# Kernel tuning notes

Hardware: AMD Instinct MI355X
Metric: run time of the kernel (lower is better)

The kernel has to match this reference:

```python
import jax, jax.numpy as jnp
import numpy as np

N_CLUSTERS = 64
MAX_ITER = 10
TOL = 1e-4


def _dists(X, C):
    """Euclidean distance matrix, shape (K, N) — mirrors torch.cdist(centroids, X, 2)."""
    x2 = jnp.sum(X * X, axis=1)            # (N,)
    c2 = jnp.sum(C * C, axis=1)            # (K,)
    d2 = c2[:, None] + x2[None, :] - 2.0 * (C @ X.T)
    return jnp.sqrt(jnp.maximum(d2, 0.0))


def _init_centroids(X):
    """KMeans++-style farthest-point init: seed with X[0], then repeatedly add the
    point farthest from the current centroid set (mirrors centroids_init)."""
    K = N_CLUSTERS
    C0 = jnp.zeros((K, X.shape[1]), X.dtype).at[0].set(X[0])

    def body(C, i):
        valid = jnp.arange(K) < i                      # slots filled so far
        d = jnp.where(valid[:, None], _dists(X, C), jnp.inf)
        min_d = jnp.min(d, axis=0)                     # dist to nearest centroid
        idx = jnp.argmax(min_d)                        # farthest point = outlier
        return C.at[i].set(X[idx]), None

    C, _ = jax.lax.scan(body, C0, jnp.arange(1, K))
    return C


def _kmeans(X):
    K = N_CLUSTERS
    C = _init_centroids(X)
    ones = jnp.ones((X.shape[0],), X.dtype)

    def step(carry, _):
        C, done = carry
        lbl = jnp.argmin(_dists(X, C), axis=0)                       # (N,)
        counts = jax.ops.segment_sum(ones, lbl, num_segments=K)      # (K,)
        sums = jax.ops.segment_sum(X, lbl, num_segments=K)           # (K, D)
        means = sums / jnp.maximum(counts, 1.0)[:, None]
        empty = counts == 0
        # Empty cluster -> re-seed with farthest point from the kept means
        # (mirrors dropping NaN rows + centroids_init re-adding an outlier).
        dm = jnp.where(empty[:, None], jnp.inf, _dists(X, means))
        far = jnp.argmax(jnp.min(dm, axis=0))
        newC = jnp.where(empty[:, None], X[far], means)
        # Shift computed only over used (non-empty) centroids, as in calc_centr_shift.
        shift = jnp.sum(jnp.where(empty[:, None], 0.0, (means - C) ** 2))
        converged = (shift <= TOL) & (~jnp.any(empty))
        newC = jnp.where(done, C, newC)                              # freeze after convergence
        return (newC, done | converged), None

    (C, _), _ = jax.lax.scan(step, (C, jnp.array(False)), None, length=MAX_ITER)
    return C


def setup_inputs() -> dict:
    key = jax.random.key(0)
    X = jax.random.normal(key, (200000, 128), dtype=jnp.float32)
    return {"X": X}


def reference(X):
    return _kmeans(X)
```

## Files before the change

kernel.cpp:

```cpp
#include <hip/hip_runtime.h>

constexpr int Dm = 128;
constexpr int D4 = 32;
constexpr int Kc = 64;
constexpr int NITER = 10;
constexpr double TOLd = 1e-4;
constexpr int BT  = 256;
constexpr int SLC = 256;
constexpr int IGB = 256;
constexpr float MARGIN = 1e-2f;

__device__ __forceinline__ float dpp_qxor_f(float v, int ctrl) {
  int t = (ctrl == 0xB1)
    ? __builtin_amdgcn_update_dpp(0, __float_as_int(v), 0xB1, 0xF, 0xF, true)
    : __builtin_amdgcn_update_dpp(0, __float_as_int(v), 0x4E, 0xF, 0xF, true);
  return __int_as_float(t);
}
__device__ __forceinline__ double dpp_qxor_d(double v, int ctrl) {
  union { double d; int i[2]; } u; u.d = v;
  int lo, hi;
  if (ctrl == 0xB1) {
    lo = __builtin_amdgcn_update_dpp(0, u.i[0], 0xB1, 0xF, 0xF, true);
    hi = __builtin_amdgcn_update_dpp(0, u.i[1], 0xB1, 0xF, 0xF, true);
  } else {
    lo = __builtin_amdgcn_update_dpp(0, u.i[0], 0x4E, 0xF, 0xF, true);
    hi = __builtin_amdgcn_update_dpp(0, u.i[1], 0x4E, 0xF, 0xF, true);
  }
  union { int i[2]; double d; } r; r.i[0] = lo; r.i[1] = hi;
  return r.d;
}

__device__ __forceinline__ void wave_argmax(double& bd, int& bi) {
#pragma unroll
  for (int off = 32; off; off >>= 1) {
    double od = __shfl_down(bd, (unsigned)off, 64);
    int    oi = __shfl_down(bi, (unsigned)off, 64);
    if (od > bd || (od == bd && oi < bi)) { bd = od; bi = oi; }
  }
}

__device__ __forceinline__ void block_argmax(double& bd, int& bi, double* wd, int* wi) {
  wave_argmax(bd, bi);
  const int w = threadIdx.x >> 6;
  if ((threadIdx.x & 63) == 0) { wd[w] = bd; wi[w] = bi; }
  __syncthreads();
  bd = wd[0]; bi = wi[0];
#pragma unroll
  for (int j = 1; j < 4; ++j) {
    double od = wd[j]; int oi = wi[j];
    if (od > bd || (od == bd && oi < bi)) { bd = od; bi = oi; }
  }
  __syncthreads();
}

__global__ __launch_bounds__(BT) void k_init_first(
    const float* __restrict__ X, float* __restrict__ Cout, double* __restrict__ Cd,
    double* __restrict__ x2d, double* __restrict__ mind,
    double* __restrict__ opd, int* __restrict__ opi, int* __restrict__ done_flag, int N) {
  __shared__ double cent[Dm];
  __shared__ double wd[4]; __shared__ int wi[4];
  const int tid = threadIdx.x;
  if (tid < Dm) cent[tid] = (double)X[tid];
  if (blockIdx.x == 0) {
    if (tid == 0) *done_flag = 0;
    if (tid < Dm) { Cout[tid] = X[tid]; Cd[tid] = (double)X[tid]; }
  }
  __syncthreads();
  double c2 = 0.0;
  for (int d = 0; d < Dm; ++d) c2 += cent[d] * cent[d];
  const int g = tid >> 2, Q = tid & 3;
  const double* cq = cent + Q * 32;
  const int STRIDE = IGB * 64;
  double bd = -1.0; int bi = 0x7fffffff;
  for (int n = blockIdx.x * 64 + g; n < N; n += STRIDE) {
    const float4* xr = (const float4*)(X + (size_t)n * Dm + Q * 32);
    double a0 = 0, a1 = 0, a2 = 0, a3 = 0;
    double x0 = 0, x1 = 0, x2 = 0, x3 = 0;
#pragma unroll
    for (int q = 0; q < 8; ++q) {
      float4 xv = xr[q];
      a0 += (double)xv.x * cq[4*q+0]; a1 += (double)xv.y * cq[4*q+1];
      a2 += (double)xv.z * cq[4*q+2]; a3 += (double)xv.w * cq[4*q+3];
      x0 += (double)xv.x * xv.x; x1 += (double)xv.y * xv.y;
      x2 += (double)xv.z * xv.z; x3 += (double)xv.w * xv.w;
    }
    double dq = (a0 + a1) + (a2 + a3);
    double d1 = dq + dpp_qxor_d(dq, 0xB1);
    double dot = d1 + dpp_qxor_d(d1, 0x4E);
    double xq = (x0 + x1) + (x2 + x3);
    double xA = xq + dpp_qxor_d(xq, 0xB1);
    double xx = xA + dpp_qxor_d(xA, 0x4E);
    if (Q == 0) {
      x2d[n] = xx;
      double d2 = c2 + xx - 2.0 * dot; if (d2 < 0.0) d2 = 0.0;
      mind[n] = d2;
      if (d2 > bd) { bd = d2; bi = n; }
    }
  }
  block_argmax(bd, bi, wd, wi);
  if (tid == 0) { opd[blockIdx.x] = bd; opi[blockIdx.x] = bi; }
}

__global__ __launch_bounds__(BT, 1) void k_init_step(
    const float* __restrict__ X, float* __restrict__ Cout, double* __restrict__ Cd,
    const double* __restrict__ x2d, double* __restrict__ mind,
    const double* __restrict__ ipd, const int* __restrict__ ipi,
    double* __restrict__ opd, int* __restrict__ opi, int N, int nparts, int ci) {
  __shared__ double cent[Dm];
  __shared__ double wd[4]; __shared__ int wi[4];
  __shared__ double s_c2;
  const int tid = threadIdx.x;
  double bd = (tid < nparts) ? ipd[tid] : -1.0;
  int    bi = (tid < nparts) ? ipi[tid] : 0x7fffffff;
  block_argmax(bd, bi, wd, wi);
  const int idx = bi;
  if (tid < Dm) {
    float v = X[(size_t)idx * Dm + tid];
    cent[tid] = (double)v;
    if (blockIdx.x == 0) {
      Cout[(size_t)ci * Dm + tid] = v;
      Cd[(size_t)ci * Dm + tid]   = (double)v;
    }
  }
  __syncthreads();
  if (tid == 0) {
    double s = 0.0;
    for (int d = 0; d < Dm; ++d) s += cent[d] * cent[d];
    s_c2 = s;
  }
  __syncthreads();
  const double c2 = s_c2;
  const int g = tid >> 2, Q = tid & 3;
  const double* cq = cent + Q * 32;
  const int STRIDE = IGB * 64;
  bd = -1.0; bi = 0x7fffffff;

  auto LOADB = [&](int n, float4* xv, double& m, double& xx) {
    const float4* xr = (const float4*)(X + (size_t)n * Dm + Q * 32);
#pragma unroll
    for (int q = 0; q < 8; ++q) xv[q] = xr[q];
    if (Q == 0) { m = mind[n]; xx = x2d[n]; }
  };
  auto PROCB = [&](int n, const float4* xv, double m, double xx) {
    double a0 = 0, a1 = 0, a2 = 0, a3 = 0;
#pragma unroll
    for (int q = 0; q < 8; ++q) {
      float4 v = xv[q];
      a0 += (double)v.x * cq[4*q+0]; a1 += (double)v.y * cq[4*q+1];
      a2 += (double)v.z * cq[4*q+2]; a3 += (double)v.w * cq[4*q+3];
    }
    double dq = (a0 + a1) + (a2 + a3);
    double d1 = dq + dpp_qxor_d(dq, 0xB1);
    double dot = d1 + dpp_qxor_d(d1, 0x4E);
    if (Q == 0) {
      double d2 = c2 + xx - 2.0 * dot; if (d2 < 0.0) d2 = 0.0;
      double mm = m; if (d2 < mm) mm = d2;
      mind[n] = mm;
      if (mm > bd) { bd = mm; bi = n; }
    }
  };

  float4 xA[8], xB[8], xC[8];
  double mA = 0, xxA = 0, mB = 0, xxB = 0, mC = 0, xxC = 0;
  int n = blockIdx.x * 64 + g;
  LOADB(n, xA, mA, xxA);
  if (n + STRIDE < N) LOADB(n + STRIDE, xB, mB, xxB);
  for (;;) {
    if (n + 2 * STRIDE < N) LOADB(n + 2 * STRIDE, xC, mC, xxC);
    PROCB(n, xA, mA, xxA);
    n += STRIDE; if (n >= N) break;
    if (n + 2 * STRIDE < N) LOADB(n + 2 * STRIDE, xA, mA, xxA);
    PROCB(n, xB, mB, xxB);
    n += STRIDE; if (n >= N) break;
    if (n + 2 * STRIDE < N) LOADB(n + 2 * STRIDE, xB, mB, xxB);
    PROCB(n, xC, mC, xxC);
    n += STRIDE; if (n >= N) break;
  }
  block_argmax(bd, bi, wd, wi);
  if (tid == 0) { opd[blockIdx.x] = bd; opi[blockIdx.x] = bi; }
}

__global__ __launch_bounds__(256) void k_pick(
    const float* __restrict__ X, float* __restrict__ Cout, double* __restrict__ Cd,
    const double* __restrict__ ipd, const int* __restrict__ ipi, int nparts, int ci,
    double* __restrict__ c2d, float* __restrict__ c2f, int* __restrict__ tie_cnt) {
  __shared__ double cent[Dm];
  __shared__ double wd[4]; __shared__ int wi[4];
  const int tid = threadIdx.x;
  double bd = (tid < nparts) ? ipd[tid] : -1.0;
  int    bi = (tid < nparts) ? ipi[tid] : 0x7fffffff;
  block_argmax(bd, bi, wd, wi);
  const int idx = bi;
  if (tid < Dm) {
    float v = X[(size_t)idx * Dm + tid];
    cent[tid] = (double)v;
    Cout[(size_t)ci * Dm + tid] = v;
    Cd[(size_t)ci * Dm + tid]   = (double)v;
  }
  __syncthreads();
  if (tid < Kc) {
    double s = 0.0;
    if (tid == ci) { for (int d = 0; d < Dm; ++d) s += cent[d] * cent[d]; }
    else { for (int d = 0; d < Dm; ++d) { double v = Cd[(size_t)tid * Dm + d]; s += v * v; } }
    c2d[tid] = s; c2f[tid] = (float)s;
  }
  if (tid == 0) *tie_cnt = 0;
}

__global__ __launch_bounds__(256, 2) void k_assign(
    const float* __restrict__ X, const float* __restrict__ Cf,
    const float* __restrict__ c2f,
    unsigned char* __restrict__ lbl,
    int* __restrict__ tie_list, int* __restrict__ tie_cnt,
    const int* __restrict__ done_flag, int N) {
  if (*done_flag) return;
  __shared__ float4 cs[Kc * 35];
  __shared__ float c2s[Kc];
  const int tid = threadIdx.x;
  for (int e = tid; e < Kc * D4; e += 256) {
    const int k = e >> 5, j = e & 31;
    cs[k * 35 + (j >> 3) * 9 + (j & 7)] = ((const float4*)Cf)[e];
  }
  if (tid < Kc) c2s[tid] = c2f[tid];
  __syncthreads();
  const int g = tid >> 2, Q = tid & 3;
  const int n0 = blockIdx.x * 256 + g * 4;
  float4 xv[4][8];
#pragma unroll
  for (int j = 0; j < 4; ++j) {
    int p = n0 + j; if (p > N - 1) p = N - 1;
    const float4* xr = (const float4*)(X + (size_t)p * Dm + Q * 32);
#pragma unroll
    for (int q = 0; q < 8; ++q) xv[j][q] = xr[q];
  }
  const float4* myc = cs + Q * 9;
  float best = 3.4028235e38f, second = 3.4028235e38f; int bk = 0;
  for (int k = 0; k < Kc; ++k) {
    const float4* ck = myc + k * 35;
    float a00=0,a01=0,a02=0,a03=0, a10=0,a11=0,a12=0,a13=0;
    float a20=0,a21=0,a22=0,a23=0, a30=0,a31=0,a32=0,a33=0;
#pragma unroll
    for (int q = 0; q < 8; ++q) {
      float4 cv = ck[q];
      a00 += xv[0][q].x*cv.x; a01 += xv[0][q].y*cv.y; a02 += xv[0][q].z*cv.z; a03 += xv[0][q].w*cv.w;
      a10 += xv[1][q].x*cv.x; a11 += xv[1][q].y*cv.y; a12 += xv[1][q].z*cv.z; a13 += xv[1][q].w*cv.w;
      a20 += xv[2][q].x*cv.x; a21 += xv[2][q].y*cv.y; a22 += xv[2][q].z*cv.z; a23 += xv[2][q].w*cv.w;
      a30 += xv[3][q].x*cv.x; a31 += xv[3][q].y*cv.y; a32 += xv[3][q].z*cv.z; a33 += xv[3][q].w*cv.w;
    }
    float d0 = (a00 + a01) + (a02 + a03);
    float d1 = (a10 + a11) + (a12 + a13);
    float d2 = (a20 + a21) + (a22 + a23);
    float d3 = (a30 + a31) + (a32 + a33);
    d0 += dpp_qxor_f(d0, 0xB1); d0 += dpp_qxor_f(d0, 0x4E);
    d1 += dpp_qxor_f(d1, 0xB1); d1 += dpp_qxor_f(d1, 0x4E);
    d2 += dpp_qxor_f(d2, 0xB1); d2 += dpp_qxor_f(d2, 0x4E);
    d3 += dpp_qxor_f(d3, 0xB1); d3 += dpp_qxor_f(d3, 0x4E);
    float mydot = (Q == 0) ? d0 : (Q == 1) ? d1 : (Q == 2) ? d2 : d3;
    float sc = c2s[k] - 2.f * mydot;
    if (sc < best) { second = best; best = sc; bk = k; }
    else if (sc < second) second = sc;
  }
  const int n = n0 + Q;
  if (n < N) {
    lbl[n] = (unsigned char)bk;
    if (second - best < MARGIN) {
      int t = atomicAdd(tie_cnt, 1);
      tie_list[t] = n;
    }
  }
}

__global__ __launch_bounds__(256) void k_tie(
    const float* __restrict__ X, const double* __restrict__ Cd,
    const double* __restrict__ c2d,
    const int* __restrict__ tie_list, const int* __restrict__ tie_cnt,
    unsigned char* __restrict__ lbl, const int* __restrict__ done_flag) {
  if (*done_flag) return;
  const int nt = *tie_cnt;
  const int gw = (int)((blockIdx.x * 256 + threadIdx.x) >> 6);
  const int lane = threadIdx.x & 63;
  const int nwaves = gridDim.x * 4;
  const double* cp = Cd + (size_t)lane * Dm;
  const double myc2 = c2d[lane];
  for (int t = gw; t < nt; t += nwaves) {
    const int n = tie_list[t];
    const float4* xr = (const float4*)(X + (size_t)n * Dm);
    double a0 = 0, a1 = 0, a2 = 0, a3 = 0;
#pragma unroll 8
    for (int q = 0; q < D4; ++q) {
      float4 xv = xr[q];
      a0 += (double)xv.x * cp[4*q+0]; a1 += (double)xv.y * cp[4*q+1];
      a2 += (double)xv.z * cp[4*q+2]; a3 += (double)xv.w * cp[4*q+3];
    }
    double sc = myc2 - 2.0 * ((a0 + a1) + (a2 + a3));
    int bk = lane;
#pragma unroll
    for (int off = 32; off; off >>= 1) {
      double osc = __shfl_down(sc, (unsigned)off, 64);
      int    obk = __shfl_down(bk, (unsigned)off, 64);
      if (osc < sc || (osc == sc && obk < bk)) { sc = osc; bk = obk; }
    }
    if (lane == 0) lbl[n] = (unsigned char)bk;
  }
}

__global__ __launch_bounds__(256) void k_sum(
    const float* __restrict__ X, const unsigned char* __restrict__ lbl,
    double* __restrict__ spart, int* __restrict__ cpart,
    const int* __restrict__ done_flag, int N, int chunk) {
  if (*done_flag) return;
  __shared__ double acc[2][Kc * Dm];
  __shared__ unsigned int sl[1024];
  __shared__ int cnt[Kc];
  const int tid = threadIdx.x;
  const int s = blockIdx.x;
  const int n0 = s * chunk;
  const int nrows = (N - n0 < chunk) ? (N - n0) : chunk;
  for (int e = tid; e < 2 * Kc * Dm; e += 256) ((double*)acc)[e] = 0.0;
  if (tid < Kc) cnt[tid] = 0;
  const int nw = (nrows > 0) ? ((nrows + 3) >> 2) : 0;
  const unsigned int* lw = (const unsigned int*)(lbl + n0);
  for (int w = tid; w < nw; w += 256) sl[w] = lw[w];
  __syncthreads();
  for (int i = tid; i < nrows; i += 256)
    atomicAdd(&cnt[(sl[i >> 2] >> ((i & 3) * 8)) & 255], 1);
  const int w = tid >> 6, L = tid & 63;
  const int parity = w >> 1, half = w & 1;
  double* ac = acc[parity] + half * 64 + L;
  const float* Xb = X + (size_t)n0 * Dm + half * 64 + L;

  auto LOADC = [&](int base, float* f, int* c) {
#pragma unroll
    for (int u = 0; u < 8; ++u) {
      const int i = base + 2 * u;
      if (i < nrows) {
        c[u] = (int)((sl[i >> 2] >> ((i & 3) * 8)) & 255u);
        f[u] = Xb[(size_t)i * Dm];
      } else c[u] = -1;
    }
  };
  auto PROCC = [&](const float* f, const int* c) {
#pragma unroll
    for (int u = 0; u < 8; ++u)
      if (c[u] >= 0) ac[c[u] * Dm] += (double)f[u];
  };

  float fA[8], fB[8], fC[8], fD[8];
  int   cA[8], cB[8], cC[8], cD[8];
  const int CS = 16;
  LOADC(parity,          fA, cA);
  LOADC(parity + CS,     fB, cB);
  LOADC(parity + 2 * CS, fC, cC);
  for (int cb = parity; cb < nrows; cb += 4 * CS) {
    LOADC(cb + 3 * CS, fD, cD); PROCC(fA, cA);
    LOADC(cb + 4 * CS, fA, cA); PROCC(fB, cB);
    LOADC(cb + 5 * CS, fB, cB); PROCC(fC, cC);
    LOADC(cb + 6 * CS, fC, cC); PROCC(fD, cD);
  }
  __syncthreads();
  for (int e = tid; e < Kc * Dm; e += 256)
    spart[(size_t)s * (Kc * Dm) + e] = acc[0][e] + acc[1][e];
  if (tid < Kc) cpart[s * Kc + tid] = cnt[tid];
}

__global__ __launch_bounds__(128) void k_update1(
    float* __restrict__ Cout, double* __restrict__ Cd,
    double* __restrict__ c2d, float* __restrict__ c2f,
    const double* __restrict__ spart, const int* __restrict__ cpart,
    double* __restrict__ shiftk, int* __restrict__ empty,
    const int* __restrict__ done_flag, int nslc) {
  if (*done_flag) return;
  __shared__ double red[128];
  __shared__ int ired[128];
  const int k = blockIdx.x, d = threadIdx.x;
  int c = 0;
  for (int s = d; s < nslc; s += 128) c += cpart[s * Kc + k];
  ired[d] = c; __syncthreads();
  for (int t = 64; t; t >>= 1) { if (d < t) ired[d] += ired[d + t]; __syncthreads(); }
  const int cnt = ired[0];
  double sum = 0.0;
#pragma unroll 8
  for (int s = 0; s < nslc; ++s) sum += spart[(size_t)s * (Kc * Dm) + k * Dm + d];
  const double mean = sum / (double)(cnt > 1 ? cnt : 1);
  const double oldv = Cd[k * Dm + d];
  Cd[k * Dm + d] = mean; Cout[k * Dm + d] = (float)mean;
  red[d] = (cnt != 0) ? (mean - oldv) * (mean - oldv) : 0.0;
  __syncthreads();
  for (int t = 64; t; t >>= 1) { if (d < t) red[d] += red[d + t]; __syncthreads(); }
  if (d == 0) shiftk[k] = red[0];
  __syncthreads();
  red[d] = mean * mean; __syncthreads();
  for (int t = 64; t; t >>= 1) { if (d < t) red[d] += red[d + t]; __syncthreads(); }
  if (d == 0) { c2d[k] = red[0]; c2f[k] = (float)red[0]; empty[k] = (cnt == 0); }
}

__global__ void k_update2(const double* __restrict__ shiftk, const int* __restrict__ empty,
                          int* __restrict__ done_flag, int* __restrict__ has_empty,
                          int* __restrict__ tie_cnt) {
  if (*done_flag) return;
  if (threadIdx.x == 0) {
    double sh = 0.0; int any = 0;
    for (int k = 0; k < Kc; ++k) { sh += shiftk[k]; any |= empty[k]; }
    *has_empty = any;
    *tie_cnt = 0;
    if (!any && sh <= TOLd) *done_flag = 1;
  }
}

__global__ __launch_bounds__(BT) void k_far(
    const float* __restrict__ X, const double* __restrict__ Cd,
    const double* __restrict__ c2d, const double* __restrict__ x2d,
    const int* __restrict__ done_flag, const int* __restrict__ has_empty,
    const int* __restrict__ empty,
    double* __restrict__ opd, int* __restrict__ opi, int N) {
  if (*done_flag || !*has_empty) return;
  __shared__ int semp[Kc];
  __shared__ double wd[4]; __shared__ int wi[4];
  if ((int)threadIdx.x < Kc) semp[threadIdx.x] = empty[threadIdx.x];
  __syncthreads();
  const int n = blockIdx.x * BT + threadIdx.x;
  double bd = -1.0; int bi = 0x7fffffff;
  if (n < N) {
    const float4* xr = (const float4*)(X + (size_t)n * Dm);
    float4 xv[D4];
#pragma unroll
    for (int q = 0; q < D4; ++q) xv[q] = xr[q];
    double md = 1e300;
    for (int k = 0; k < Kc; ++k) {
      if (semp[k]) continue;
      double a0 = 0, a1 = 0, a2 = 0, a3 = 0;
      const double* cp = Cd + (size_t)k * Dm;
#pragma unroll
      for (int q = 0; q < D4; ++q) {
        a0 += (double)xv[q].x * cp[4*q+0]; a1 += (double)xv[q].y * cp[4*q+1];
        a2 += (double)xv[q].z * cp[4*q+2]; a3 += (double)xv[q].w * cp[4*q+3];
      }
      double d2v = c2d[k] + x2d[n] - 2.0 * ((a0 + a1) + (a2 + a3));
      if (d2v < 0.0) d2v = 0.0;
      if (d2v < md) md = d2v;
    }
    bd = md; bi = n;
  }
  block_argmax(bd, bi, wd, wi);
  if (threadIdx.x == 0) { opd[blockIdx.x] = bd; opi[blockIdx.x] = bi; }
}

__global__ __launch_bounds__(BT) void k_fix(
    const float* __restrict__ X, float* __restrict__ Cout, double* __restrict__ Cd,
    double* __restrict__ c2d, float* __restrict__ c2f,
    const int* __restrict__ done_flag, const int* __restrict__ has_empty,
    const int* __restrict__ empty,
    const double* __restrict__ ipd, const int* __restrict__ ipi, int nparts) {
  if (*done_flag || !*has_empty) return;
  const int lane = threadIdx.x & 63;
  double bd = -1.0; int bi = 0x7fffffff;
  for (int t = lane; t < nparts; t += 64) {
    double d = ipd[t]; int id = ipi[t];
    if (d > bd || (d == bd && id < bi)) { bd = d; bi = id; }
  }
  wave_argmax(bd, bi);
  const int far = __shfl(bi, 0, 64);
  for (int e = threadIdx.x; e < Kc * Dm; e += BT) {
    if (empty[e >> 7]) {
      float v = X[(size_t)far * Dm + (e & 127)];
      Cout[e] = v; Cd[e] = (double)v;
    }
  }
  __syncthreads();
  if ((int)threadIdx.x < Kc && empty[threadIdx.x]) {
    double s2 = 0.0;
    for (int d = 0; d < Dm; ++d) { double v = Cd[(size_t)threadIdx.x * Dm + d]; s2 += v * v; }
    c2d[threadIdx.x] = s2; c2f[threadIdx.x] = (float)s2;
  }
}

extern "C" void kernel_launch(void* const* d_in, const int* in_sizes, int n_in,
                              void* d_out, int out_size, void* d_ws, size_t ws_size,
                              hipStream_t stream) {
  const float* X = (const float*)d_in[0];
  const int N = in_sizes[0] / Dm;
  float* Cout = (float*)d_out;
  (void)ws_size; (void)n_in; (void)out_size;

  char* w = (char*)d_ws;
  auto alloc = [&](size_t bytes) -> void* {
    void* p = (void*)w; w += (bytes + 255) & ~(size_t)255; return p;
  };
  const size_t NP = ((size_t)N + 255) & ~(size_t)255;
  const int IB  = (N + BT - 1) / BT;
  const int ABL = (N + 255) / 256;
  double* x2d  = (double*)alloc(NP * 8);
  const size_t spart_bytes = (size_t)SLC * Kc * Dm * 8;
  const size_t union_bytes = (spart_bytes > NP * 8) ? spart_bytes : NP * 8;
  double* mind  = (double*)alloc(union_bytes);
  double* spart = mind;
  double* pd0  = (double*)alloc(4096 * 8);
  double* pd1  = (double*)alloc(4096 * 8);
  int*    pi0  = (int*)alloc(4096 * 4);
  int*    pi1  = (int*)alloc(4096 * 4);
  double* Cd   = (double*)alloc((size_t)Kc * Dm * 8);
  double* c2d  = (double*)alloc(Kc * 8);
  float*  c2f  = (float*)alloc(Kc * 4);
  int*    cpart = (int*)alloc(SLC * Kc * 4);
  double* shiftk = (double*)alloc(Kc * 8);
  unsigned char* lbl = (unsigned char*)alloc(NP);
  int*    tie_list = (int*)alloc(NP * 4);
  int*    tie_cnt  = (int*)alloc(4);
  int*    done  = (int*)alloc(4);
  int*    hasem = (int*)alloc(4);
  int*    empty = (int*)alloc(Kc * 4);

  double* pd[2] = {pd0, pd1};
  int*    pi[2] = {pi0, pi1};

  k_init_first<<<IGB, BT, 0, stream>>>(X, Cout, Cd, x2d, mind, pd[0], pi[0], done, N);
  for (int i = 1; i <= 62; ++i) {
    const int rb = (i + 1) & 1, wb = i & 1;
    k_init_step<<<IGB, BT, 0, stream>>>(X, Cout, Cd, x2d, mind, pd[rb], pi[rb],
                                        pd[wb], pi[wb], N, IGB, i);
  }
  k_pick<<<1, 256, 0, stream>>>(X, Cout, Cd, pd[0], pi[0], IGB, 63,
                                c2d, c2f, tie_cnt);

  const int chunk = ((N + SLC - 1) / SLC + 3) & ~3;
  for (int it = 0; it < NITER; ++it) {
    k_assign<<<ABL, 256, 0, stream>>>(X, Cout, c2f, lbl, tie_list, tie_cnt, done, N);
    k_tie<<<128, 256, 0, stream>>>(X, Cd, c2d, tie_list, tie_cnt, lbl, done);
    k_sum<<<SLC, 256, 0, stream>>>(X, lbl, spart, cpart, done, N, chunk);
    k_update1<<<Kc, 128, 0, stream>>>(Cout, Cd, c2d, c2f, spart, cpart,
                                      shiftk, empty, done, SLC);
    k_update2<<<1, 64, 0, stream>>>(shiftk, empty, done, hasem, tie_cnt);
    k_far<<<IB, BT, 0, stream>>>(X, Cd, c2d, x2d, done, hasem, empty, pd0, pi0, N);
    k_fix<<<1, BT, 0, stream>>>(X, Cout, Cd, c2d, c2f, done, hasem, empty, pd0, pi0, IB);
  }
}
```

Measured before the change: 3.395 ms.

## Screen init farthest-point distances with an fp16 copy of X, refine in fp64

```diff
diff --git a/kernel.cpp b/kernel.cpp
--- a/kernel.cpp
+++ b/kernel.cpp
@@ -1,4 +1,5 @@
 #include <hip/hip_runtime.h>
+#include <hip/hip_fp16.h>
 
 constexpr int Dm = 128;
 constexpr int D4 = 32;
@@ -7,8 +8,9 @@
 constexpr double TOLd = 1e-4;
 constexpr int BT  = 256;
 constexpr int SLC = 256;
-constexpr int IGB = 256;
+constexpr int IGB = 512;
 constexpr float MARGIN = 1e-2f;
+constexpr double IMARG = 4.0;
 
 __device__ __forceinline__ float dpp_qxor_f(float v, int ctrl) {
   int t = (ctrl == 0xB1)
@@ -51,6 +53,21 @@
     if (od > bd || (od == bd && oi < bi)) { bd = od; bi = oi; }
   }
   __syncthreads();
+}
+
+__global__ __launch_bounds__(256) void k_prep(
+    const float4* __restrict__ X4, uint4* __restrict__ Xh4, int ntot8) {
+  const int gid = blockIdx.x * 256 + threadIdx.x;
+  if (gid >= ntot8) return;
+  float4 a = X4[gid * 2], b = X4[gid * 2 + 1];
+  __half2 h0 = __floats2half2_rn(a.x, a.y);
+  __half2 h1 = __floats2half2_rn(a.z, a.w);
+  __half2 h2 = __floats2half2_rn(b.x, b.y);
+  __half2 h3 = __floats2half2_rn(b.z, b.w);
+  uint4 o;
+  o.x = *(unsigned int*)&h0; o.y = *(unsigned int*)&h1;
+  o.z = *(unsigned int*)&h2; o.w = *(unsigned int*)&h3;
+  Xh4[gid] = o;
 }
 
 __global__ __launch_bounds__(BT) void k_init_first(
@@ -101,6 +118,108 @@
   if (tid == 0) { opd[blockIdx.x] = bd; opi[blockIdx.x] = bi; }
 }
 
+__global__ __launch_bounds__(BT, 2) void k_init_step_h(
+    const float* __restrict__ X, const __half* __restrict__ Xh,
+    float* __restrict__ Cout, double* __restrict__ Cd,
+    const double* __restrict__ x2d, double* __restrict__ mind,
+    const double* __restrict__ ipd, const int* __restrict__ ipi,
+    double* __restrict__ opd, int* __restrict__ opi, int N, int nparts, int ci) {
+  __shared__ double cent[Dm];
+  __shared__ float centf[Dm];
+  __shared__ double wd[4]; __shared__ int wi[4];
+  __shared__ double s_c2;
+  const int tid = threadIdx.x;
+  double bd = -1.0; int bi = 0x7fffffff;
+  for (int t = tid; t < nparts; t += BT) {
+    double d = ipd[t]; int id = ipi[t];
+    if (d > bd || (d == bd && id < bi)) { bd = d; bi = id; }
+  }
+  block_argmax(bd, bi, wd, wi);
+  const int idx = bi;
+  if (tid < Dm) {
+    float v = X[(size_t)idx * Dm + tid];
+    cent[tid]  = (double)v;
+    centf[tid] = v;
+    if (blockIdx.x == 0) {
+      Cout[(size_t)ci * Dm + tid] = v;
+      Cd[(size_t)ci * Dm + tid]   = (double)v;
+    }
+  }
+  __syncthreads();
+  if (tid == 0) {
+    double s = 0.0;
+    for (int d = 0; d < Dm; ++d) s += cent[d] * cent[d];
+    s_c2 = s;
+  }
+  __syncthreads();
+  const double c2 = s_c2;
+  const int g = tid >> 2, Q = tid & 3;
+  const double* cq = cent + Q * 32;
+  const float2* cf2 = (const float2*)(centf + Q * 32);
+  const int STRIDE = IGB * 64;
+  bd = -1.0; bi = 0x7fffffff;
+
+  auto LOADH = [&](int n, uint4* h, double& m, double& xx) {
+    const uint4* hr = (const uint4*)(Xh + (size_t)n * Dm + Q * 32);
+#pragma unroll
+    for (int q = 0; q < 4; ++q) h[q] = hr[q];
+    m = mind[n]; xx = x2d[n];
+  };
+  auto PROCH = [&](int n, const uint4* h, double m, double xx) {
+    float a0 = 0.f, a1 = 0.f;
+#pragma unroll
+    for (int j = 0; j < 4; ++j) {
+      union { uint4 u; __half2 p[4]; } U; U.u = h[j];
+#pragma unroll
+      for (int t = 0; t < 4; ++t) {
+        float2 xf = __half22float2(U.p[t]);
+        float2 c  = cf2[j * 4 + t];
+        a0 = fmaf(xf.x, c.x, a0); a1 = fmaf(xf.y, c.y, a1);
+      }
+    }
+    float dq = a0 + a1;
+    dq += dpp_qxor_f(dq, 0xB1); dq += dpp_qxor_f(dq, 0x4E);
+    const double ds = c2 + xx - 2.0 * (double)dq;
+    double mm = m;
+    if (!(ds - m > IMARG)) {
+      const float4* xr = (const float4*)(X + (size_t)n * Dm + Q * 32);
+      double b0 = 0, b1 = 0, b2 = 0, b3 = 0;
+#pragma unroll
+      for (int q = 0; q < 8; ++q) {
+        float4 v = xr[q];
+        b0 += (double)v.x * cq[4*q+0]; b1 += (double)v.y * cq[4*q+1];
+        b2 += (double)v.z * cq[4*q+2]; b3 += (double)v.w * cq[4*q+3];
+      }
+      double dqd = (b0 + b1) + (b2 + b3);
+      double d1 = dqd + dpp_qxor_d(dqd, 0xB1);
+      double dot = d1 + dpp_qxor_d(d1, 0x4E);
+      double d2v = c2 + xx - 2.0 * dot; if (d2v < 0.0) d2v = 0.0;
+      if (d2v < mm) mm = d2v;
+      if (Q == 0) mind[n] = mm;
+    }
+    if (Q == 0 && mm > bd) { bd = mm; bi = n; }
+  };
+
+  uint4 hA[4], hB[4];
+  double mA = 0, xxA = 0, mB = 0, xxB = 0;
+  int n = blockIdx.x * 64 + g;
+  if (n < N) {
+    LOADH(n, hA, mA, xxA);
+    for (;;) {
+      int nn = n + STRIDE;
+      if (nn < N) LOADH(nn, hB, mB, xxB);
+      PROCH(n, hA, mA, xxA);
+      n = nn; if (n >= N) break;
+      nn = n + STRIDE;
+      if (nn < N) LOADH(nn, hA, mA, xxA);
+      PROCH(n, hB, mB, xxB);
+      n = nn; if (n >= N) break;
+    }
+  }
+  block_argmax(bd, bi, wd, wi);
+  if (tid == 0) { opd[blockIdx.x] = bd; opi[blockIdx.x] = bi; }
+}
+
 __global__ __launch_bounds__(BT, 1) void k_init_step(
     const float* __restrict__ X, float* __restrict__ Cout, double* __restrict__ Cd,
     const double* __restrict__ x2d, double* __restrict__ mind,
@@ -110,8 +229,11 @@
   __shared__ double wd[4]; __shared__ int wi[4];
   __shared__ double s_c2;
   const int tid = threadIdx.x;
-  double bd = (tid < nparts) ? ipd[tid] : -1.0;
-  int    bi = (tid < nparts) ? ipi[tid] : 0x7fffffff;
+  double bd = -1.0; int bi = 0x7fffffff;
+  for (int t = tid; t < nparts; t += BT) {
+    double d = ipd[t]; int id = ipi[t];
+    if (d > bd || (d == bd && id < bi)) { bd = d; bi = id; }
+  }
   block_argmax(bd, bi, wd, wi);
   const int idx = bi;
   if (tid < Dm) {
@@ -134,7 +256,6 @@
   const double* cq = cent + Q * 32;
   const int STRIDE = IGB * 64;
   bd = -1.0; bi = 0x7fffffff;
-
   auto LOADB = [&](int n, float4* xv, double& m, double& xx) {
     const float4* xr = (const float4*)(X + (size_t)n * Dm + Q * 32);
 #pragma unroll
@@ -159,22 +280,23 @@
       if (mm > bd) { bd = mm; bi = n; }
     }
   };
-
   float4 xA[8], xB[8], xC[8];
   double mA = 0, xxA = 0, mB = 0, xxB = 0, mC = 0, xxC = 0;
   int n = blockIdx.x * 64 + g;
-  LOADB(n, xA, mA, xxA);
-  if (n + STRIDE < N) LOADB(n + STRIDE, xB, mB, xxB);
-  for (;;) {
-    if (n + 2 * STRIDE < N) LOADB(n + 2 * STRIDE, xC, mC, xxC);
-    PROCB(n, xA, mA, xxA);
-    n += STRIDE; if (n >= N) break;
-    if (n + 2 * STRIDE < N) LOADB(n + 2 * STRIDE, xA, mA, xxA);
-    PROCB(n, xB, mB, xxB);
-    n += STRIDE; if (n >= N) break;
-    if (n + 2 * STRIDE < N) LOADB(n + 2 * STRIDE, xB, mB, xxB);
-    PROCB(n, xC, mC, xxC);
-    n += STRIDE; if (n >= N) break;
+  if (n < N) {
+    LOADB(n, xA, mA, xxA);
+    if (n + STRIDE < N) LOADB(n + STRIDE, xB, mB, xxB);
+    for (;;) {
+      if (n + 2 * STRIDE < N) LOADB(n + 2 * STRIDE, xC, mC, xxC);
+      PROCB(n, xA, mA, xxA);
+      n += STRIDE; if (n >= N) break;
+      if (n + 2 * STRIDE < N) LOADB(n + 2 * STRIDE, xA, mA, xxA);
+      PROCB(n, xB, mB, xxB);
+      n += STRIDE; if (n >= N) break;
+      if (n + 2 * STRIDE < N) LOADB(n + 2 * STRIDE, xB, mB, xxB);
+      PROCB(n, xC, mC, xxC);
+      n += STRIDE; if (n >= N) break;
+    }
   }
   block_argmax(bd, bi, wd, wi);
   if (tid == 0) { opd[blockIdx.x] = bd; opi[blockIdx.x] = bi; }
@@ -187,8 +309,11 @@
   __shared__ double cent[Dm];
   __shared__ double wd[4]; __shared__ int wi[4];
   const int tid = threadIdx.x;
-  double bd = (tid < nparts) ? ipd[tid] : -1.0;
-  int    bi = (tid < nparts) ? ipi[tid] : 0x7fffffff;
+  double bd = -1.0; int bi = 0x7fffffff;
+  for (int t = tid; t < nparts; t += 256) {
+    double d = ipd[t]; int id = ipi[t];
+    if (d > bd || (d == bd && id < bi)) { bd = d; bi = id; }
+  }
   block_argmax(bd, bi, wd, wi);
   const int idx = bi;
   if (tid < Dm) {
@@ -328,7 +453,6 @@
   const int parity = w >> 1, half = w & 1;
   double* ac = acc[parity] + half * 64 + L;
   const float* Xb = X + (size_t)n0 * Dm + half * 64 + L;
-
   auto LOADC = [&](int base, float* f, int* c) {
 #pragma unroll
     for (int u = 0; u < 8; ++u) {
@@ -344,7 +468,6 @@
     for (int u = 0; u < 8; ++u)
       if (c[u] >= 0) ac[c[u] * Dm] += (double)f[u];
   };
-
   float fA[8], fB[8], fC[8], fD[8];
   int   cA[8], cB[8], cC[8], cD[8];
   const int CS = 16;
@@ -480,7 +603,7 @@
   const float* X = (const float*)d_in[0];
   const int N = in_sizes[0] / Dm;
   float* Cout = (float*)d_out;
-  (void)ws_size; (void)n_in; (void)out_size;
+  (void)n_in; (void)out_size;
 
   char* w = (char*)d_ws;
   auto alloc = [&](size_t bytes) -> void* {
@@ -509,15 +632,25 @@
   int*    done  = (int*)alloc(4);
   int*    hasem = (int*)alloc(4);
   int*    empty = (int*)alloc(Kc * 4);
+  __half* Xh = (__half*)alloc((size_t)N * Dm * 2);
+  const bool use_h = ((size_t)(w - (char*)d_ws) <= ws_size);
 
   double* pd[2] = {pd0, pd1};
   int*    pi[2] = {pi0, pi1};
 
+  if (use_h) {
+    const int ntot8 = N * Dm / 8;
+    k_prep<<<(ntot8 + 255) / 256, 256, 0, stream>>>((const float4*)X, (uint4*)Xh, ntot8);
+  }
   k_init_first<<<IGB, BT, 0, stream>>>(X, Cout, Cd, x2d, mind, pd[0], pi[0], done, N);
   for (int i = 1; i <= 62; ++i) {
     const int rb = (i + 1) & 1, wb = i & 1;
-    k_init_step<<<IGB, BT, 0, stream>>>(X, Cout, Cd, x2d, mind, pd[rb], pi[rb],
-                                        pd[wb], pi[wb], N, IGB, i);
+    if (use_h)
+      k_init_step_h<<<IGB, BT, 0, stream>>>(X, Xh, Cout, Cd, x2d, mind, pd[rb], pi[rb],
+                                            pd[wb], pi[wb], N, IGB, i);
+    else
+      k_init_step<<<IGB, BT, 0, stream>>>(X, Cout, Cd, x2d, mind, pd[rb], pi[rb],
+                                          pd[wb], pi[wb], N, IGB, i);
   }
   k_pick<<<1, 256, 0, stream>>>(X, Cout, Cd, pd[0], pi[0], IGB, 63,
                                 c2d, c2f, tie_cnt);
```

Measured after the change: 3.012 ms. -11.3%, faster.
